# Kernel optimization log

Hardware: AMD Instinct MI355X
Metric: run time of the kernel (lower is better)

## Reference

```python
import jax, jax.numpy as jnp
import numpy as np

N_NODES = 100000
N_EDGES = 3200000
F_IN = 128
NOUT = 32


def _lin(x, W, b):
    return x @ W + b


def _spect_conv(x, src, dst, W, b, n_nodes):
    # edge_attr is all-ones with a single frequency (K=1), so SpectConv reduces to
    # an unweighted scatter-add of linearly transformed source-node features.
    h = x @ W                                   # [N, nout]
    agg = jax.ops.segment_sum(h[src], dst, num_segments=n_nodes)  # [N, nout]
    return agg + b


def setup_inputs() -> dict:
    key = jax.random.key(0)
    ks = jax.random.split(key, 32)
    s = 0.05

    def w(k, shape):
        return jax.random.normal(k, shape, dtype=jnp.float32) * s

    inp = {
        "x": jax.random.normal(ks[0], (N_NODES, F_IN), dtype=jnp.float32),
        "edge_index": jax.random.randint(ks[1], (2, N_EDGES), 0, N_NODES, dtype=jnp.int32),
        # SpectConv weights (single frequency) + biases
        "Wc1": w(ks[2], (F_IN, NOUT)), "bc1": jnp.zeros((NOUT,), jnp.float32),
        "Wc2": w(ks[3], (NOUT, NOUT)), "bc2": jnp.zeros((NOUT,), jnp.float32),
        "Wc3": w(ks[4], (NOUT, NOUT)), "bc3": jnp.zeros((NOUT,), jnp.float32),
        # dense branch weights
        "W11": w(ks[5], (F_IN, NOUT)), "b11": w(ks[6], (NOUT,)),
        "W12": w(ks[7], (F_IN, NOUT)), "b12": w(ks[8], (NOUT,)),
        "W13": w(ks[9], (F_IN, NOUT)), "b13": w(ks[10], (NOUT,)),
        "W21": w(ks[11], (NOUT, NOUT)), "b21": w(ks[12], (NOUT,)),
        "W22": w(ks[13], (NOUT, NOUT)), "b22": w(ks[14], (NOUT,)),
        "W23": w(ks[15], (NOUT, NOUT)), "b23": w(ks[16], (NOUT,)),
        "W31": w(ks[17], (NOUT, NOUT)), "b31": w(ks[18], (NOUT,)),
        "W32": w(ks[19], (NOUT, NOUT)), "b32": w(ks[20], (NOUT,)),
        "W33": w(ks[21], (NOUT, NOUT)), "b33": w(ks[22], (NOUT,)),
        "W2": w(ks[23], (NOUT, 1)), "b2": w(ks[24], (1,)),
    }
    return inp


def reference(x, edge_index,
              Wc1, bc1, Wc2, bc2, Wc3, bc3,
              W11, b11, W12, b12, W13, b13,
              W21, b21, W22, b22, W23, b23,
              W31, b31, W32, b32, W33, b33,
              W2, b2):
    src, dst = edge_index[0], edge_index[1]
    n = x.shape[0]
    relu = jax.nn.relu

    def block(h, Wa, ba, Wc, bc, Wm1, bm1, Wm2, bm2):
        return (relu(_lin(h, Wa, ba))
                + relu(_spect_conv(h, src, dst, Wc, bc, n))
                + relu(_lin(h, Wm1, bm1) * _lin(h, Wm2, bm2)))

    h = block(x, W11, b11, Wc1, bc1, W12, b12, W13, b13)
    h = block(h, W21, b21, Wc2, bc2, W22, b22, W23, b23)
    h = block(h, W31, b31, Wc3, bc3, W32, b32, W33, b33)
    return _lin(h, W2, b2)
```

## Files before the change

kernel.cpp:

```cpp
#include <hip/hip_runtime.h>
#include <hip/hip_bf16.h>

#define N_FEAT 32
#define CBITS 7
#define CAP   6000
#define TILE  8192

typedef __attribute__((ext_vector_type(8))) short short8;
typedef __attribute__((ext_vector_type(4))) float floatx4;

static __device__ __forceinline__ unsigned short f2b(float f) {
    unsigned u = __float_as_uint(f);
    return (unsigned short)((u + 0x7FFFu + ((u >> 16) & 1u)) >> 16);
}
static __device__ __forceinline__ float b2f(unsigned short b) {
    return __uint_as_float(((unsigned)b) << 16);
}

template <int K, bool BF16_IN>
__global__ __launch_bounds__(256)
void transform_mfma_kernel(const void* __restrict__ hin,
                           const float* __restrict__ Wa, const float* __restrict__ ba,
                           const float* __restrict__ Wc,
                           const float* __restrict__ Wm1, const float* __restrict__ bm1,
                           const float* __restrict__ Wm2, const float* __restrict__ bm2,
                           unsigned short* __restrict__ t_pre, unsigned short* __restrict__ t_c,
                           int n_nodes)
{
    constexpr int WPITCH = (K == 32) ? 40 : 136;
    __shared__ unsigned short sW[128][WPITCH];

    const int t = threadIdx.x;
    const int node0 = blockIdx.x * 64;
    const int wave = t >> 6;
    const int lane = t & 63;
    const int m16 = lane & 15;
    const int quad = lane >> 4;

    for (int i = t; i < 128 * K; i += 256) {
        const int c = i & 127, kk = i >> 7;
        const int mat = c >> 5, cl = c & 31;
        const float* W = (mat == 0) ? Wa : (mat == 1) ? Wc : (mat == 2) ? Wm1 : Wm2;
        sW[c][kk] = f2b(W[(size_t)kk * 32 + cl]);
    }
    __syncthreads();

    const int n = node0 + wave * 16 + m16;
    const bool nok = (n < n_nodes);

    floatx4 acc[8];
#pragma unroll
    for (int i = 0; i < 8; ++i) acc[i] = (floatx4){0.f, 0.f, 0.f, 0.f};

#pragma unroll
    for (int k0 = 0; k0 < K; k0 += 32) {
        short8 a;
        if (BF16_IN) {
            const unsigned short* hb = (const unsigned short*)hin;
            a = nok ? *reinterpret_cast<const short8*>(hb + (size_t)n * K + k0 + quad * 8)
                    : (short8){0,0,0,0,0,0,0,0};
        } else {
            const float* hf = (const float*)hin;
            if (nok) {
                const float4 v0 = *reinterpret_cast<const float4*>(hf + (size_t)n * K + k0 + quad * 8);
                const float4 v1 = *reinterpret_cast<const float4*>(hf + (size_t)n * K + k0 + quad * 8 + 4);
                union { short8 v; unsigned short u[8]; } pk;
                pk.u[0] = f2b(v0.x); pk.u[1] = f2b(v0.y); pk.u[2] = f2b(v0.z); pk.u[3] = f2b(v0.w);
                pk.u[4] = f2b(v1.x); pk.u[5] = f2b(v1.y); pk.u[6] = f2b(v1.z); pk.u[7] = f2b(v1.w);
                a = pk.v;
            } else {
                a = (short8){0,0,0,0,0,0,0,0};
            }
        }
#pragma unroll
        for (int t8 = 0; t8 < 8; ++t8) {
            const short8 b = *reinterpret_cast<const short8*>(&sW[t8 * 16 + m16][k0 + quad * 8]);
            acc[t8] = __builtin_amdgcn_mfma_f32_16x16x32_bf16(a, b, acc[t8], 0, 0, 0);
        }
    }

#pragma unroll
    for (int r = 0; r < 4; ++r) {
        const int node = node0 + wave * 16 + quad * 4 + r;
        if (node < n_nodes) {
#pragma unroll
            for (int half = 0; half < 2; ++half) {
                const int c = m16 + half * 16;
                const float av  = acc[0 + half][r] + ba[c];
                const float wcv = acc[2 + half][r];
                const float m1  = acc[4 + half][r] + bm1[c];
                const float m2  = acc[6 + half][r] + bm2[c];
                t_pre[(size_t)node * N_FEAT + c] = f2b(fmaxf(av, 0.f) + fmaxf(m1 * m2, 0.f));
                t_c[(size_t)node * N_FEAT + c] = f2b(wcv);
            }
        }
    }
}

__global__ __launch_bounds__(1024)
void coarse_bin_kernel(const int* __restrict__ src, const int* __restrict__ dst,
                       unsigned* __restrict__ cnt_g, unsigned* __restrict__ binned,
                       int n_edges, int n_buckets)
{
    __shared__ unsigned sorted[TILE];
    __shared__ unsigned hist[1024];
    __shared__ unsigned lbase[1024];
    __shared__ unsigned gofs[1024];
    __shared__ unsigned part[1024];

    const int t = threadIdx.x;
    const int e0 = blockIdx.x * TILE;
    const int cnt = min(TILE, n_edges - e0);
    if (cnt <= 0) return;

    hist[t] = 0;
    __syncthreads();
    for (int i = t; i < cnt; i += 1024)
        atomicAdd(&hist[(unsigned)dst[e0 + i] >> CBITS], 1u);
    __syncthreads();

    const unsigned myh = hist[t];
    part[t] = myh;
    __syncthreads();
    for (int off = 1; off < 1024; off <<= 1) {
        const unsigned v = (t >= off) ? part[t - off] : 0u;
        __syncthreads();
        part[t] += v;
        __syncthreads();
    }
    lbase[t] = part[t] - myh;
    __syncthreads();

    if (t < n_buckets) {
        const unsigned h = hist[t];
        gofs[t] = h ? atomicAdd(&cnt_g[t], h) : 0u;
    }
    hist[t] = 0;
    __syncthreads();

    for (int i = t; i < cnt; i += 1024) {
        const unsigned d = (unsigned)dst[e0 + i];
        const unsigned s = (unsigned)src[e0 + i];
        const unsigned b = d >> CBITS;
        const unsigned pos = lbase[b] + atomicAdd(&hist[b], 1u);
        sorted[pos] = ((d & ((1u << CBITS) - 1)) << 17) | s;
    }
    __syncthreads();

    if (t < n_buckets) {
        const unsigned lb = lbase[t], n = hist[t], g0 = gofs[t];
        for (unsigned j = 0; j < n; ++j) {
            const unsigned gp = g0 + j;
            if (gp < CAP) binned[(size_t)t * CAP + gp] = sorted[lb + j];
        }
    }
}

__global__ __launch_bounds__(1024)
void bucket_scan_kernel(const unsigned* __restrict__ cnt_g,
                        unsigned* __restrict__ obase, int n_buckets)
{
    __shared__ unsigned part[1024];
    const int t = threadIdx.x;
    part[t] = (t < n_buckets) ? min(cnt_g[t], (unsigned)CAP) : 0u;
    __syncthreads();
    for (int off = 1; off < 1024; off <<= 1) {
        const unsigned v = (t >= off) ? part[t - off] : 0u;
        __syncthreads();
        part[t] += v;
        __syncthreads();
    }
    if (t < n_buckets) obase[t] = (t == 0) ? 0u : part[t - 1];
}

__global__ __launch_bounds__(512)
void fine_sort_kernel(const unsigned* __restrict__ binned,
                      const unsigned* __restrict__ cnt_g,
                      const unsigned* __restrict__ obase,
                      int* __restrict__ srcs, unsigned* __restrict__ rowptr,
                      int n_nodes, int n_buckets)
{
    __shared__ int sorted_src[CAP];
    __shared__ unsigned hist[512];
    __shared__ unsigned incl[512];
    __shared__ unsigned ebase[512];

    const int t = threadIdx.x;
    const int b = blockIdx.x;
    const unsigned cnt = min(cnt_g[b], (unsigned)CAP);
    const unsigned ob = obase[b];
    const int node0 = b << CBITS;
    const int nodes_here = min(128, n_nodes - node0);
    const unsigned* tile = binned + (size_t)b * CAP;

    hist[t] = 0;
    __syncthreads();
    for (unsigned i = t; i < cnt; i += 512) {
        const unsigned e = tile[i];
        atomicAdd(&hist[((e >> 17) << 2) | ((e & 0x1FFFFu) >> 15)], 1u);
    }
    __syncthreads();

    const unsigned myh = hist[t];
    incl[t] = myh;
    __syncthreads();
    for (int off = 1; off < 512; off <<= 1) {
        const unsigned v = (t >= off) ? incl[t - off] : 0u;
        __syncthreads();
        incl[t] += v;
        __syncthreads();
    }
    ebase[t] = incl[t] - myh;
    __syncthreads();

    if (t < nodes_here) rowptr[node0 + t] = ob + ebase[t << 2];
    if (b == n_buckets - 1 && t == 0) rowptr[n_nodes] = ob + cnt;

    hist[t] = 0;
    __syncthreads();
    for (unsigned i = t; i < cnt; i += 512) {
        const unsigned e = tile[i];
        const unsigned key = ((e >> 17) << 2) | ((e & 0x1FFFFu) >> 15);
        const unsigned pos = ebase[key] + atomicAdd(&hist[key], 1u);
        sorted_src[pos] = (int)(e & 0x1FFFFu);
    }
    __syncthreads();
    for (unsigned i = t; i < cnt; i += 512)
        srcs[ob + i] = sorted_src[i];
}

static __device__ __forceinline__ void add8(float* a, short8 v) {
#pragma unroll
    for (int j = 0; j < 8; ++j) a[j] += b2f((unsigned short)v[j]);
}

__global__ __launch_bounds__(256)
void gather_combine_kernel(const unsigned short* __restrict__ t_c,
                           const unsigned short* __restrict__ t_pre,
                           const unsigned* __restrict__ rowptr, const int* __restrict__ srcs,
                           const float* __restrict__ bc, unsigned short* __restrict__ hout,
                           int n_nodes)
{
    const int node = blockIdx.x * 64 + (threadIdx.x >> 2);
    const int l4 = threadIdx.x & 3;
    const int f0 = l4 * 8;
    if (node >= n_nodes) return;
    const unsigned lo = rowptr[node], hi = rowptr[node + 1];
    float acc[8] = {0.f, 0.f, 0.f, 0.f, 0.f, 0.f, 0.f, 0.f};
    unsigned i = lo;
    for (; i + 4 <= hi; i += 4) {
        const int s0 = srcs[i], s1 = srcs[i+1], s2 = srcs[i+2], s3 = srcs[i+3];
        const short8 v0 = *reinterpret_cast<const short8*>(t_c + (size_t)s0 * N_FEAT + f0);
        const short8 v1 = *reinterpret_cast<const short8*>(t_c + (size_t)s1 * N_FEAT + f0);
        const short8 v2 = *reinterpret_cast<const short8*>(t_c + (size_t)s2 * N_FEAT + f0);
        const short8 v3 = *reinterpret_cast<const short8*>(t_c + (size_t)s3 * N_FEAT + f0);
        add8(acc, v0); add8(acc, v1); add8(acc, v2); add8(acc, v3);
    }
    for (; i < hi; ++i)
        add8(acc, *reinterpret_cast<const short8*>(t_c + (size_t)srcs[i] * N_FEAT + f0));

    const short8 p = *reinterpret_cast<const short8*>(t_pre + (size_t)node * N_FEAT + f0);
    union { short8 v; unsigned short u[8]; } r;
#pragma unroll
    for (int j = 0; j < 8; ++j)
        r.u[j] = f2b(b2f((unsigned short)p[j]) + fmaxf(acc[j] + bc[f0 + j], 0.f));
    *reinterpret_cast<short8*>(hout + (size_t)node * N_FEAT + f0) = r.v;
}

__global__ __launch_bounds__(256)
void gather_final_kernel(const unsigned short* __restrict__ t_c,
                         const unsigned short* __restrict__ t_pre,
                         const unsigned* __restrict__ rowptr, const int* __restrict__ srcs,
                         const float* __restrict__ bc, const float* __restrict__ W2,
                         const float* __restrict__ b2, float* __restrict__ out,
                         int n_nodes)
{
    const int node = blockIdx.x * 64 + (threadIdx.x >> 2);
    const int l4 = threadIdx.x & 3;
    const int f0 = l4 * 8;
    if (node >= n_nodes) return;
    const unsigned lo = rowptr[node], hi = rowptr[node + 1];
    float acc[8] = {0.f, 0.f, 0.f, 0.f, 0.f, 0.f, 0.f, 0.f};
    unsigned i = lo;
    for (; i + 4 <= hi; i += 4) {
        const int s0 = srcs[i], s1 = srcs[i+1], s2 = srcs[i+2], s3 = srcs[i+3];
        const short8 v0 = *reinterpret_cast<const short8*>(t_c + (size_t)s0 * N_FEAT + f0);
        const short8 v1 = *reinterpret_cast<const short8*>(t_c + (size_t)s1 * N_FEAT + f0);
        const short8 v2 = *reinterpret_cast<const short8*>(t_c + (size_t)s2 * N_FEAT + f0);
        const short8 v3 = *reinterpret_cast<const short8*>(t_c + (size_t)s3 * N_FEAT + f0);
        add8(acc, v0); add8(acc, v1); add8(acc, v2); add8(acc, v3);
    }
    for (; i < hi; ++i)
        add8(acc, *reinterpret_cast<const short8*>(t_c + (size_t)srcs[i] * N_FEAT + f0));

    const short8 p = *reinterpret_cast<const short8*>(t_pre + (size_t)node * N_FEAT + f0);
    float r = 0.f;
#pragma unroll
    for (int j = 0; j < 8; ++j)
        r += (b2f((unsigned short)p[j]) + fmaxf(acc[j] + bc[f0 + j], 0.f)) * W2[f0 + j];
    r += __shfl_down(r, 2, 4);
    r += __shfl_down(r, 1, 4);
    if (l4 == 0) out[node] = r + b2[0];
}

extern "C" void kernel_launch(void* const* d_in, const int* in_sizes, int n_in,
                              void* d_out, int out_size, void* d_ws, size_t ws_size,
                              hipStream_t stream)
{
    const float* x   = (const float*)d_in[0];
    const int*   ei  = (const int*)d_in[1];
    const float* Wc1 = (const float*)d_in[2];  const float* bc1 = (const float*)d_in[3];
    const float* Wc2 = (const float*)d_in[4];  const float* bc2 = (const float*)d_in[5];
    const float* Wc3 = (const float*)d_in[6];  const float* bc3 = (const float*)d_in[7];
    const float* W11 = (const float*)d_in[8];  const float* b11 = (const float*)d_in[9];
    const float* W12 = (const float*)d_in[10]; const float* b12 = (const float*)d_in[11];
    const float* W13 = (const float*)d_in[12]; const float* b13 = (const float*)d_in[13];
    const float* W21 = (const float*)d_in[14]; const float* b21 = (const float*)d_in[15];
    const float* W22 = (const float*)d_in[16]; const float* b22 = (const float*)d_in[17];
    const float* W23 = (const float*)d_in[18]; const float* b23 = (const float*)d_in[19];
    const float* W31 = (const float*)d_in[20]; const float* b31 = (const float*)d_in[21];
    const float* W32 = (const float*)d_in[22]; const float* b32 = (const float*)d_in[23];
    const float* W33 = (const float*)d_in[24]; const float* b33 = (const float*)d_in[25];
    const float* W2  = (const float*)d_in[26]; const float* b2  = (const float*)d_in[27];

    const int n_nodes = in_sizes[0] / 128;
    const int n_edges = in_sizes[1] / 2;
    const int* src = ei;
    const int* dst = ei + n_edges;
    const int n_buckets = (n_nodes + (1 << CBITS) - 1) >> CBITS;

    const size_t feat_elems = (size_t)n_nodes * N_FEAT;

    unsigned short* tpre   = (unsigned short*)d_ws;
    unsigned short* tc     = tpre + feat_elems;
    unsigned short* hbuf   = tc + feat_elems;
    int*            srcs   = (int*)(hbuf + feat_elems);
    unsigned*       rowptr = (unsigned*)(srcs + n_edges);
    unsigned*       cnt_g  = rowptr + (n_nodes + 1);
    unsigned*       obase  = cnt_g + n_buckets;
    unsigned*       binned = (unsigned*)d_ws;

    const int tf_grid  = (n_nodes + 63) / 64;
    const int gc_grid  = (n_nodes + 63) / 64;
    const int cb_grid  = (n_edges + TILE - 1) / TILE;

    hipMemsetAsync(cnt_g, 0, (size_t)n_buckets * sizeof(unsigned), stream);
    coarse_bin_kernel<<<cb_grid, 1024, 0, stream>>>(src, dst, cnt_g, binned, n_edges, n_buckets);
    bucket_scan_kernel<<<1, 1024, 0, stream>>>(cnt_g, obase, n_buckets);
    fine_sort_kernel<<<n_buckets, 512, 0, stream>>>(binned, cnt_g, obase, srcs, rowptr,
                                                    n_nodes, n_buckets);

    transform_mfma_kernel<128, false><<<tf_grid, 256, 0, stream>>>(
        x, W11, b11, Wc1, W12, b12, W13, b13, tpre, tc, n_nodes);
    gather_combine_kernel<<<gc_grid, 256, 0, stream>>>(tc, tpre, rowptr, srcs, bc1, hbuf, n_nodes);

    transform_mfma_kernel<32, true><<<tf_grid, 256, 0, stream>>>(
        hbuf, W21, b21, Wc2, W22, b22, W23, b23, tpre, tc, n_nodes);
    gather_combine_kernel<<<gc_grid, 256, 0, stream>>>(tc, tpre, rowptr, srcs, bc2, hbuf, n_nodes);

    transform_mfma_kernel<32, true><<<tf_grid, 256, 0, stream>>>(
        hbuf, W31, b31, Wc3, W32, b32, W33, b33, tpre, tc, n_nodes);
    gather_final_kernel<<<gc_grid, 256, 0, stream>>>(tc, tpre, rowptr, srcs, bc3, W2, b2,
                                                     (float*)d_out, n_nodes);
}
```

Before: 352.4 us.

## Fuse first-layer transform with edge binning and drop the bucket scan kernel

Merges the layer-1 MFMA transform and the coarse edge-binning pass into one heterogeneous launch, with a block-index split and a shared-memory union, so the two independent stages run concurrently. The bucket prefix-scan kernel is removed: each fine-sort block grabs its output base with a global atomic, and per-node rowstart/rowend replace the contiguous rowptr. Buckets are therefore laid out in arbitrary order. The gather loops are also unrolled to 8 outstanding loads. The binned buffer moves so it no longer aliases the transform outputs, which adds workspace use. The coarse tile and block sizes are also reduced.

```diff
diff --git a/kernel.cpp b/kernel.cpp
--- a/kernel.cpp
+++ b/kernel.cpp
@@ -4,7 +4,7 @@
 #define N_FEAT 32
 #define CBITS 7
 #define CAP   6000
-#define TILE  8192
+#define CTILE 4096
 
 typedef __attribute__((ext_vector_type(8))) short short8;
 typedef __attribute__((ext_vector_type(4))) float floatx4;
@@ -17,18 +17,156 @@
     return __uint_as_float(((unsigned)b) << 16);
 }
 
-template <int K, bool BF16_IN>
+struct CoarseS {
+    unsigned sorted[CTILE];
+    unsigned hist[1024];
+    unsigned lbase[1024];
+    unsigned gofs[1024];
+    unsigned part[512];
+};
+union FatS {
+    unsigned short sW[128][136];
+    CoarseS s;
+};
+
+__global__ __launch_bounds__(512)
+void fused_transform_sort_kernel(const float* __restrict__ x,
+                                 const float* __restrict__ Wa, const float* __restrict__ ba,
+                                 const float* __restrict__ Wc,
+                                 const float* __restrict__ Wm1, const float* __restrict__ bm1,
+                                 const float* __restrict__ Wm2, const float* __restrict__ bm2,
+                                 unsigned short* __restrict__ t_pre,
+                                 unsigned short* __restrict__ t_c,
+                                 int n_nodes, int tf_grid,
+                                 const int* __restrict__ src, const int* __restrict__ dst,
+                                 unsigned* __restrict__ cnt_g, unsigned* __restrict__ binned,
+                                 int n_edges, int n_buckets)
+{
+    __shared__ FatS u;
+    const int t = threadIdx.x;
+
+    if ((int)blockIdx.x < tf_grid) {
+        constexpr int K = 128;
+        const int node0 = blockIdx.x * 128;
+        const int wave = t >> 6;
+        const int lane = t & 63;
+        const int m16 = lane & 15;
+        const int quad = lane >> 4;
+
+        for (int i = t; i < 128 * K; i += 512) {
+            const int c = i & 127, kk = i >> 7;
+            const int mat = c >> 5, cl = c & 31;
+            const float* W = (mat == 0) ? Wa : (mat == 1) ? Wc : (mat == 2) ? Wm1 : Wm2;
+            u.sW[c][kk] = f2b(W[(size_t)kk * 32 + cl]);
+        }
+        __syncthreads();
+
+        const int n = node0 + wave * 16 + m16;
+        const bool nok = (n < n_nodes);
+
+        floatx4 acc[8];
+#pragma unroll
+        for (int i = 0; i < 8; ++i) acc[i] = (floatx4){0.f, 0.f, 0.f, 0.f};
+
+#pragma unroll
+        for (int k0 = 0; k0 < K; k0 += 32) {
+            short8 a;
+            if (nok) {
+                const float4 v0 = *reinterpret_cast<const float4*>(x + (size_t)n * K + k0 + quad * 8);
+                const float4 v1 = *reinterpret_cast<const float4*>(x + (size_t)n * K + k0 + quad * 8 + 4);
+                union { short8 v; unsigned short uu[8]; } pk;
+                pk.uu[0] = f2b(v0.x); pk.uu[1] = f2b(v0.y); pk.uu[2] = f2b(v0.z); pk.uu[3] = f2b(v0.w);
+                pk.uu[4] = f2b(v1.x); pk.uu[5] = f2b(v1.y); pk.uu[6] = f2b(v1.z); pk.uu[7] = f2b(v1.w);
+                a = pk.v;
+            } else {
+                a = (short8){0,0,0,0,0,0,0,0};
+            }
+#pragma unroll
+            for (int t8 = 0; t8 < 8; ++t8) {
+                const short8 b = *reinterpret_cast<const short8*>(&u.sW[t8 * 16 + m16][k0 + quad * 8]);
+                acc[t8] = __builtin_amdgcn_mfma_f32_16x16x32_bf16(a, b, acc[t8], 0, 0, 0);
+            }
+        }
+
+#pragma unroll
+        for (int r = 0; r < 4; ++r) {
+            const int node = node0 + wave * 16 + quad * 4 + r;
+            if (node < n_nodes) {
+#pragma unroll
+                for (int half = 0; half < 2; ++half) {
+                    const int c = m16 + half * 16;
+                    const float av  = acc[0 + half][r] + ba[c];
+                    const float wcv = acc[2 + half][r];
+                    const float m1  = acc[4 + half][r] + bm1[c];
+                    const float m2  = acc[6 + half][r] + bm2[c];
+                    t_pre[(size_t)node * N_FEAT + c] = f2b(fmaxf(av, 0.f) + fmaxf(m1 * m2, 0.f));
+                    t_c[(size_t)node * N_FEAT + c] = f2b(wcv);
+                }
+            }
+        }
+    } else {
+        CoarseS& s = u.s;
+        const int blk = blockIdx.x - tf_grid;
+        const int e0 = blk * CTILE;
+        const int cnt = min(CTILE, n_edges - e0);
+        if (cnt <= 0) return;
+
+        for (int i = t; i < 1024; i += 512) s.hist[i] = 0;
+        __syncthreads();
+        for (int i = t; i < cnt; i += 512)
+            atomicAdd(&s.hist[(unsigned)dst[e0 + i] >> CBITS], 1u);
+        __syncthreads();
+
+        const unsigned c0 = s.hist[2 * t], c1 = s.hist[2 * t + 1];
+        s.part[t] = c0 + c1;
+        __syncthreads();
+        for (int off = 1; off < 512; off <<= 1) {
+            const unsigned v = (t >= off) ? s.part[t - off] : 0u;
+            __syncthreads();
+            s.part[t] += v;
+            __syncthreads();
+        }
+        const unsigned base = (t == 0) ? 0u : s.part[t - 1];
+        s.lbase[2 * t] = base;
+        s.lbase[2 * t + 1] = base + c0;
+
+        for (int i = t; i < n_buckets; i += 512) {
+            const unsigned h = s.hist[i];
+            s.gofs[i] = h ? atomicAdd(&cnt_g[i], h) : 0u;
+        }
+        for (int i = t; i < 1024; i += 512) s.hist[i] = 0;
+        __syncthreads();
+
+        for (int i = t; i < cnt; i += 512) {
+            const unsigned d = (unsigned)dst[e0 + i];
+            const unsigned sv = (unsigned)src[e0 + i];
+            const unsigned b = d >> CBITS;
+            const unsigned pos = s.lbase[b] + atomicAdd(&s.hist[b], 1u);
+            s.sorted[pos] = ((d & ((1u << CBITS) - 1)) << 17) | sv;
+        }
+        __syncthreads();
+
+        for (int i = t; i < n_buckets; i += 512) {
+            const unsigned lb = s.lbase[i], n = s.hist[i], g0 = s.gofs[i];
+            for (unsigned j = 0; j < n; ++j) {
+                const unsigned gp = g0 + j;
+                if (gp < CAP) binned[(size_t)i * CAP + gp] = s.sorted[lb + j];
+            }
+        }
+    }
+}
+
 __global__ __launch_bounds__(256)
-void transform_mfma_kernel(const void* __restrict__ hin,
-                           const float* __restrict__ Wa, const float* __restrict__ ba,
-                           const float* __restrict__ Wc,
-                           const float* __restrict__ Wm1, const float* __restrict__ bm1,
-                           const float* __restrict__ Wm2, const float* __restrict__ bm2,
-                           unsigned short* __restrict__ t_pre, unsigned short* __restrict__ t_c,
-                           int n_nodes)
-{
-    constexpr int WPITCH = (K == 32) ? 40 : 136;
-    __shared__ unsigned short sW[128][WPITCH];
+void transform32_kernel(const unsigned short* __restrict__ hin,
+                        const float* __restrict__ Wa, const float* __restrict__ ba,
+                        const float* __restrict__ Wc,
+                        const float* __restrict__ Wm1, const float* __restrict__ bm1,
+                        const float* __restrict__ Wm2, const float* __restrict__ bm2,
+                        unsigned short* __restrict__ t_pre, unsigned short* __restrict__ t_c,
+                        int n_nodes)
+{
+    constexpr int K = 32;
+    __shared__ unsigned short sW[128][40];
 
     const int t = threadIdx.x;
     const int node0 = blockIdx.x * 64;
@@ -52,31 +190,12 @@
 #pragma unroll
     for (int i = 0; i < 8; ++i) acc[i] = (floatx4){0.f, 0.f, 0.f, 0.f};
 
-#pragma unroll
-    for (int k0 = 0; k0 < K; k0 += 32) {
-        short8 a;
-        if (BF16_IN) {
-            const unsigned short* hb = (const unsigned short*)hin;
-            a = nok ? *reinterpret_cast<const short8*>(hb + (size_t)n * K + k0 + quad * 8)
-                    : (short8){0,0,0,0,0,0,0,0};
-        } else {
-            const float* hf = (const float*)hin;
-            if (nok) {
-                const float4 v0 = *reinterpret_cast<const float4*>(hf + (size_t)n * K + k0 + quad * 8);
-                const float4 v1 = *reinterpret_cast<const float4*>(hf + (size_t)n * K + k0 + quad * 8 + 4);
-                union { short8 v; unsigned short u[8]; } pk;
-                pk.u[0] = f2b(v0.x); pk.u[1] = f2b(v0.y); pk.u[2] = f2b(v0.z); pk.u[3] = f2b(v0.w);
-                pk.u[4] = f2b(v1.x); pk.u[5] = f2b(v1.y); pk.u[6] = f2b(v1.z); pk.u[7] = f2b(v1.w);
-                a = pk.v;
-            } else {
-                a = (short8){0,0,0,0,0,0,0,0};
-            }
-        }
-#pragma unroll
-        for (int t8 = 0; t8 < 8; ++t8) {
-            const short8 b = *reinterpret_cast<const short8*>(&sW[t8 * 16 + m16][k0 + quad * 8]);
-            acc[t8] = __builtin_amdgcn_mfma_f32_16x16x32_bf16(a, b, acc[t8], 0, 0, 0);
-        }
+    const short8 a = nok ? *reinterpret_cast<const short8*>(hin + (size_t)n * K + quad * 8)
+                         : (short8){0,0,0,0,0,0,0,0};
+#pragma unroll
+    for (int t8 = 0; t8 < 8; ++t8) {
+        const short8 b = *reinterpret_cast<const short8*>(&sW[t8 * 16 + m16][quad * 8]);
+        acc[t8] = __builtin_amdgcn_mfma_f32_16x16x32_bf16(a, b, acc[t8], 0, 0, 0);
     }
 
 #pragma unroll
@@ -97,104 +216,32 @@
     }
 }
 
-__global__ __launch_bounds__(1024)
-void coarse_bin_kernel(const int* __restrict__ src, const int* __restrict__ dst,
-                       unsigned* __restrict__ cnt_g, unsigned* __restrict__ binned,
-                       int n_edges, int n_buckets)
-{
-    __shared__ unsigned sorted[TILE];
-    __shared__ unsigned hist[1024];
-    __shared__ unsigned lbase[1024];
-    __shared__ unsigned gofs[1024];
-    __shared__ unsigned part[1024];
-
-    const int t = threadIdx.x;
-    const int e0 = blockIdx.x * TILE;
-    const int cnt = min(TILE, n_edges - e0);
-    if (cnt <= 0) return;
-
-    hist[t] = 0;
-    __syncthreads();
-    for (int i = t; i < cnt; i += 1024)
-        atomicAdd(&hist[(unsigned)dst[e0 + i] >> CBITS], 1u);
-    __syncthreads();
-
-    const unsigned myh = hist[t];
-    part[t] = myh;
-    __syncthreads();
-    for (int off = 1; off < 1024; off <<= 1) {
-        const unsigned v = (t >= off) ? part[t - off] : 0u;
-        __syncthreads();
-        part[t] += v;
-        __syncthreads();
-    }
-    lbase[t] = part[t] - myh;
-    __syncthreads();
-
-    if (t < n_buckets) {
-        const unsigned h = hist[t];
-        gofs[t] = h ? atomicAdd(&cnt_g[t], h) : 0u;
-    }
-    hist[t] = 0;
-    __syncthreads();
-
-    for (int i = t; i < cnt; i += 1024) {
-        const unsigned d = (unsigned)dst[e0 + i];
-        const unsigned s = (unsigned)src[e0 + i];
-        const unsigned b = d >> CBITS;
-        const unsigned pos = lbase[b] + atomicAdd(&hist[b], 1u);
-        sorted[pos] = ((d & ((1u << CBITS) - 1)) << 17) | s;
-    }
-    __syncthreads();
-
-    if (t < n_buckets) {
-        const unsigned lb = lbase[t], n = hist[t], g0 = gofs[t];
-        for (unsigned j = 0; j < n; ++j) {
-            const unsigned gp = g0 + j;
-            if (gp < CAP) binned[(size_t)t * CAP + gp] = sorted[lb + j];
-        }
-    }
-}
-
-__global__ __launch_bounds__(1024)
-void bucket_scan_kernel(const unsigned* __restrict__ cnt_g,
-                        unsigned* __restrict__ obase, int n_buckets)
-{
-    __shared__ unsigned part[1024];
-    const int t = threadIdx.x;
-    part[t] = (t < n_buckets) ? min(cnt_g[t], (unsigned)CAP) : 0u;
-    __syncthreads();
-    for (int off = 1; off < 1024; off <<= 1) {
-        const unsigned v = (t >= off) ? part[t - off] : 0u;
-        __syncthreads();
-        part[t] += v;
-        __syncthreads();
-    }
-    if (t < n_buckets) obase[t] = (t == 0) ? 0u : part[t - 1];
-}
-
 __global__ __launch_bounds__(512)
 void fine_sort_kernel(const unsigned* __restrict__ binned,
                       const unsigned* __restrict__ cnt_g,
-                      const unsigned* __restrict__ obase,
-                      int* __restrict__ srcs, unsigned* __restrict__ rowptr,
+                      unsigned* __restrict__ total_ctr,
+                      int* __restrict__ srcs,
+                      unsigned* __restrict__ rowstart, unsigned* __restrict__ rowend,
                       int n_nodes, int n_buckets)
 {
     __shared__ int sorted_src[CAP];
     __shared__ unsigned hist[512];
     __shared__ unsigned incl[512];
     __shared__ unsigned ebase[512];
+    __shared__ unsigned ob_s;
 
     const int t = threadIdx.x;
     const int b = blockIdx.x;
     const unsigned cnt = min(cnt_g[b], (unsigned)CAP);
-    const unsigned ob = obase[b];
     const int node0 = b << CBITS;
     const int nodes_here = min(128, n_nodes - node0);
     const unsigned* tile = binned + (size_t)b * CAP;
 
+    if (t == 0) ob_s = atomicAdd(total_ctr, cnt);
     hist[t] = 0;
     __syncthreads();
+    const unsigned ob = ob_s;
+
     for (unsigned i = t; i < cnt; i += 512) {
         const unsigned e = tile[i];
         atomicAdd(&hist[((e >> 17) << 2) | ((e & 0x1FFFFu) >> 15)], 1u);
@@ -213,8 +260,10 @@
     ebase[t] = incl[t] - myh;
     __syncthreads();
 
-    if (t < nodes_here) rowptr[node0 + t] = ob + ebase[t << 2];
-    if (b == n_buckets - 1 && t == 0) rowptr[n_nodes] = ob + cnt;
+    if (t < nodes_here) {
+        rowstart[node0 + t] = ob + ebase[t << 2];
+        rowend[node0 + t]   = ob + incl[(t << 2) + 3];
+    }
 
     hist[t] = 0;
     __syncthreads();
@@ -237,7 +286,9 @@
 __global__ __launch_bounds__(256)
 void gather_combine_kernel(const unsigned short* __restrict__ t_c,
                            const unsigned short* __restrict__ t_pre,
-                           const unsigned* __restrict__ rowptr, const int* __restrict__ srcs,
+                           const unsigned* __restrict__ rowstart,
+                           const unsigned* __restrict__ rowend,
+                           const int* __restrict__ srcs,
                            const float* __restrict__ bc, unsigned short* __restrict__ hout,
                            int n_nodes)
 {
@@ -245,16 +296,24 @@
     const int l4 = threadIdx.x & 3;
     const int f0 = l4 * 8;
     if (node >= n_nodes) return;
-    const unsigned lo = rowptr[node], hi = rowptr[node + 1];
+    const unsigned lo = rowstart[node], hi = rowend[node];
     float acc[8] = {0.f, 0.f, 0.f, 0.f, 0.f, 0.f, 0.f, 0.f};
     unsigned i = lo;
+    for (; i + 8 <= hi; i += 8) {
+        short8 v[8];
+#pragma unroll
+        for (int j = 0; j < 8; ++j)
+            v[j] = *reinterpret_cast<const short8*>(t_c + (size_t)srcs[i + j] * N_FEAT + f0);
+#pragma unroll
+        for (int j = 0; j < 8; ++j) add8(acc, v[j]);
+    }
     for (; i + 4 <= hi; i += 4) {
-        const int s0 = srcs[i], s1 = srcs[i+1], s2 = srcs[i+2], s3 = srcs[i+3];
-        const short8 v0 = *reinterpret_cast<const short8*>(t_c + (size_t)s0 * N_FEAT + f0);
-        const short8 v1 = *reinterpret_cast<const short8*>(t_c + (size_t)s1 * N_FEAT + f0);
-        const short8 v2 = *reinterpret_cast<const short8*>(t_c + (size_t)s2 * N_FEAT + f0);
-        const short8 v3 = *reinterpret_cast<const short8*>(t_c + (size_t)s3 * N_FEAT + f0);
-        add8(acc, v0); add8(acc, v1); add8(acc, v2); add8(acc, v3);
+        short8 v[4];
+#pragma unroll
+        for (int j = 0; j < 4; ++j)
+            v[j] = *reinterpret_cast<const short8*>(t_c + (size_t)srcs[i + j] * N_FEAT + f0);
+#pragma unroll
+        for (int j = 0; j < 4; ++j) add8(acc, v[j]);
     }
     for (; i < hi; ++i)
         add8(acc, *reinterpret_cast<const short8*>(t_c + (size_t)srcs[i] * N_FEAT + f0));
@@ -270,7 +329,9 @@
 __global__ __launch_bounds__(256)
 void gather_final_kernel(const unsigned short* __restrict__ t_c,
                          const unsigned short* __restrict__ t_pre,
-                         const unsigned* __restrict__ rowptr, const int* __restrict__ srcs,
+                         const unsigned* __restrict__ rowstart,
+                         const unsigned* __restrict__ rowend,
+                         const int* __restrict__ srcs,
                          const float* __restrict__ bc, const float* __restrict__ W2,
                          const float* __restrict__ b2, float* __restrict__ out,
                          int n_nodes)
@@ -279,16 +340,24 @@
     const int l4 = threadIdx.x & 3;
     const int f0 = l4 * 8;
     if (node >= n_nodes) return;
-    const unsigned lo = rowptr[node], hi = rowptr[node + 1];
+    const unsigned lo = rowstart[node], hi = rowend[node];
     float acc[8] = {0.f, 0.f, 0.f, 0.f, 0.f, 0.f, 0.f, 0.f};
     unsigned i = lo;
+    for (; i + 8 <= hi; i += 8) {
+        short8 v[8];
+#pragma unroll
+        for (int j = 0; j < 8; ++j)
+            v[j] = *reinterpret_cast<const short8*>(t_c + (size_t)srcs[i + j] * N_FEAT + f0);
+#pragma unroll
+        for (int j = 0; j < 8; ++j) add8(acc, v[j]);
+    }
     for (; i + 4 <= hi; i += 4) {
-        const int s0 = srcs[i], s1 = srcs[i+1], s2 = srcs[i+2], s3 = srcs[i+3];
-        const short8 v0 = *reinterpret_cast<const short8*>(t_c + (size_t)s0 * N_FEAT + f0);
-        const short8 v1 = *reinterpret_cast<const short8*>(t_c + (size_t)s1 * N_FEAT + f0);
-        const short8 v2 = *reinterpret_cast<const short8*>(t_c + (size_t)s2 * N_FEAT + f0);
-        const short8 v3 = *reinterpret_cast<const short8*>(t_c + (size_t)s3 * N_FEAT + f0);
-        add8(acc, v0); add8(acc, v1); add8(acc, v2); add8(acc, v3);
+        short8 v[4];
+#pragma unroll
+        for (int j = 0; j < 4; ++j)
+            v[j] = *reinterpret_cast<const short8*>(t_c + (size_t)srcs[i + j] * N_FEAT + f0);
+#pragma unroll
+        for (int j = 0; j < 4; ++j) add8(acc, v[j]);
     }
     for (; i < hi; ++i)
         add8(acc, *reinterpret_cast<const short8*>(t_c + (size_t)srcs[i] * N_FEAT + f0));
@@ -331,35 +400,38 @@
 
     const size_t feat_elems = (size_t)n_nodes * N_FEAT;
 
-    unsigned short* tpre   = (unsigned short*)d_ws;
-    unsigned short* tc     = tpre + feat_elems;
-    unsigned short* hbuf   = tc + feat_elems;
-    int*            srcs   = (int*)(hbuf + feat_elems);
-    unsigned*       rowptr = (unsigned*)(srcs + n_edges);
-    unsigned*       cnt_g  = rowptr + (n_nodes + 1);
-    unsigned*       obase  = cnt_g + n_buckets;
-    unsigned*       binned = (unsigned*)d_ws;
-
-    const int tf_grid  = (n_nodes + 63) / 64;
-    const int gc_grid  = (n_nodes + 63) / 64;
-    const int cb_grid  = (n_edges + TILE - 1) / TILE;
-
-    hipMemsetAsync(cnt_g, 0, (size_t)n_buckets * sizeof(unsigned), stream);
-    coarse_bin_kernel<<<cb_grid, 1024, 0, stream>>>(src, dst, cnt_g, binned, n_edges, n_buckets);
-    bucket_scan_kernel<<<1, 1024, 0, stream>>>(cnt_g, obase, n_buckets);
-    fine_sort_kernel<<<n_buckets, 512, 0, stream>>>(binned, cnt_g, obase, srcs, rowptr,
-                                                    n_nodes, n_buckets);
-
-    transform_mfma_kernel<128, false><<<tf_grid, 256, 0, stream>>>(
-        x, W11, b11, Wc1, W12, b12, W13, b13, tpre, tc, n_nodes);
-    gather_combine_kernel<<<gc_grid, 256, 0, stream>>>(tc, tpre, rowptr, srcs, bc1, hbuf, n_nodes);
-
-    transform_mfma_kernel<32, true><<<tf_grid, 256, 0, stream>>>(
+    unsigned short* tpre     = (unsigned short*)d_ws;
+    unsigned short* tc       = tpre + feat_elems;
+    unsigned short* hbuf     = tc + feat_elems;
+    int*            srcs     = (int*)(hbuf + feat_elems);
+    unsigned*       rowstart = (unsigned*)(srcs + n_edges);
+    unsigned*       rowend   = rowstart + n_nodes;
+    unsigned*       cnt_g    = rowend + n_nodes;
+    unsigned*       binned   = cnt_g + (n_buckets + 1);
+
+    const int tf_grid128 = (n_nodes + 127) / 128;
+    const int cb_grid    = (n_edges + CTILE - 1) / CTILE;
+    const int tf_grid64  = (n_nodes + 63) / 64;
+    const int gc_grid    = (n_nodes + 63) / 64;
+
+    hipMemsetAsync(cnt_g, 0, ((size_t)n_buckets + 1) * sizeof(unsigned), stream);
+    fused_transform_sort_kernel<<<tf_grid128 + cb_grid, 512, 0, stream>>>(
+        x, W11, b11, Wc1, W12, b12, W13, b13, tpre, tc, n_nodes, tf_grid128,
+        src, dst, cnt_g, binned, n_edges, n_buckets);
+
+    fine_sort_kernel<<<n_buckets, 512, 0, stream>>>(
+        binned, cnt_g, cnt_g + n_buckets, srcs, rowstart, rowend, n_nodes, n_buckets);
+
+    gather_combine_kernel<<<gc_grid, 256, 0, stream>>>(
+        tc, tpre, rowstart, rowend, srcs, bc1, hbuf, n_nodes);
+
+    transform32_kernel<<<tf_grid64, 256, 0, stream>>>(
         hbuf, W21, b21, Wc2, W22, b22, W23, b23, tpre, tc, n_nodes);
-    gather_combine_kernel<<<gc_grid, 256, 0, stream>>>(tc, tpre, rowptr, srcs, bc2, hbuf, n_nodes);
-
-    transform_mfma_kernel<32, true><<<tf_grid, 256, 0, stream>>>(
+    gather_combine_kernel<<<gc_grid, 256, 0, stream>>>(
+        tc, tpre, rowstart, rowend, srcs, bc2, hbuf, n_nodes);
+
+    transform32_kernel<<<tf_grid64, 256, 0, stream>>>(
         hbuf, W31, b31, Wc3, W32, b32, W33, b33, tpre, tc, n_nodes);
-    gather_final_kernel<<<gc_grid, 256, 0, stream>>>(tc, tpre, rowptr, srcs, bc3, W2, b2,
-                                                     (float*)d_out, n_nodes);
-}
+    gather_final_kernel<<<gc_grid, 256, 0, stream>>>(
+        tc, tpre, rowstart, rowend, srcs, bc3, W2, b2, (float*)d_out, n_nodes);
+}
```

Measured after the change: 348.8 us. About the same (-1.0%).
